# Optimization experiments

Hardware: AMD Instinct MI355X
Metric: run time of the kernel (lower is better)

The kernel has to match this reference:

```python
import jax, jax.numpy as jnp
import numpy as np

VOCAB, D = 10000, 32
QUEUE_LEN = 100


def setup_inputs() -> dict:
    key = jax.random.key(0)
    ks = jax.random.split(key, 8)
    B, T = 64, 1024
    s = 0.1
    return dict(
        inputs=jax.random.randint(ks[0], (B, T), 0, 10000, dtype=jnp.int32),
        emb=jax.random.normal(ks[1], (VOCAB, D), dtype=jnp.float32) * s,
        k_lstm=jax.random.normal(ks[2], (D, 4 * D), dtype=jnp.float32) * s,
        rk_lstm=jax.random.normal(ks[3], (D, 4 * D), dtype=jnp.float32) * s,
        b_lstm=jnp.zeros((4 * D,), dtype=jnp.float32),
        W1=jax.random.normal(ks[4], (D, D), dtype=jnp.float32) * s,
        b1=jnp.zeros((D,), dtype=jnp.float32),
        W2=jax.random.normal(ks[5], (D, 1), dtype=jnp.float32) * s,
        b2=jnp.zeros((1,), dtype=jnp.float32),
    )


def _lstm(x, k, rk, b):
    # Keras LSTM, gate order [i, f, g(cell), o], sigmoid recurrent act, tanh act.
    B, T, D = x.shape
    xg = jnp.einsum('btd,de->bte', x, k) + b  # precompute input projections

    def step(carry, xg_t):
        h, c = carry
        z = xg_t + h @ rk
        i, f, g, o = jnp.split(z, 4, axis=-1)
        c = jax.nn.sigmoid(f) * c + jax.nn.sigmoid(i) * jnp.tanh(g)
        h = jax.nn.sigmoid(o) * jnp.tanh(c)
        return (h, c), h

    init = (jnp.zeros((B, D), x.dtype), jnp.zeros((B, D), x.dtype))
    _, hs = jax.lax.scan(step, init, jnp.swapaxes(xg, 0, 1))  # [T,B,D]
    return jnp.swapaxes(hs, 0, 1)  # [B,T,D]


def _zero_index_queue(x_ids):
    # Vectorized replacement of the (i,j) Python scan: last QUEUE_LEN positions
    # (row-major order) where token==0, as [QUEUE_LEN,2] int32, padded with -1.
    B, T = x_ids.shape
    flat = (x_ids == 0).reshape(-1)
    N = flat.shape[0]
    ridx = jnp.nonzero(flat[::-1], size=QUEUE_LEN, fill_value=-1)[0]
    pos = jnp.where(ridx >= 0, N - 1 - ridx, -1)[::-1]  # ascending, like deque
    ii = jnp.where(pos >= 0, pos // T, -1)
    jj = jnp.where(pos >= 0, pos % T, -1)
    return jnp.stack([ii, jj], axis=-1).astype(jnp.int32)


def _forward_float(x_ids, emb, k_lstm, rk_lstm, b_lstm, W1, b1, W2, b2):
    x = emb[x_ids]                                  # [B,T,D]
    h = _lstm(x, k_lstm, rk_lstm, b_lstm)           # [B,T,D]
    scores = jnp.einsum('btd,bsd->bts', h, h)       # unscaled dot attention
    attn = jax.nn.softmax(scores, axis=-1)
    ctx = jnp.einsum('bts,bsd->btd', attn, h)       # Keras Attention output
    y = jnp.einsum('btd,bte->bde', ctx, h)          # Dot(axes=(1,1)) -> [B,D,D]
    y = jax.nn.relu(y @ W1 + b1)
    return jax.nn.sigmoid(y @ W2 + b2)              # [B,D,1]


def reference(inputs, emb, k_lstm, rk_lstm, b_lstm, W1, b1, W2, b2):
    x_ids = jnp.where(inputs < VOCAB, inputs, 0)
    out = _forward_float(x_ids, emb, k_lstm, rk_lstm, b_lstm, W1, b1, W2, b2)
    return out, _zero_index_queue(x_ids)
```

## Files before the change

kernel.cpp:

```cpp
#include <hip/hip_runtime.h>
#include <math.h>

#define BB 64
#define TT 1024
#define DD 32
#define GG 128
#define VOCABN 10000
#define QLEN 100

typedef short short8 __attribute__((ext_vector_type(8)));
typedef float floatx4 __attribute__((ext_vector_type(4)));
typedef float floatx2 __attribute__((ext_vector_type(2)));
typedef unsigned short u16;

__device__ __forceinline__ float fsig(float x) {
    return __builtin_amdgcn_rcpf(1.0f + __expf(-x));
}
__device__ __forceinline__ float readlane_f(float v, int l) {
    return __int_as_float(__builtin_amdgcn_readlane(__float_as_int(v), l));
}
__device__ __forceinline__ u16 f2bf_rne(float x) {
    unsigned u = __float_as_uint(x);
    u += 0x7FFF + ((u >> 16) & 1);
    return (u16)(u >> 16);
}
__device__ __forceinline__ float bf2f(u16 s) {
    return __uint_as_float(((unsigned)s) << 16);
}
__device__ __forceinline__ floatx2 fma2(float s, floatx2 w, floatx2 acc) {
    return __builtin_elementwise_fma((floatx2){s, s}, w, acc);
}

#define UU 8
__global__
__attribute__((amdgpu_flat_work_group_size(128, 128)))
__attribute__((amdgpu_waves_per_eu(1, 1)))
void k_lstm_scan(const int* __restrict__ ids,
                 const float* __restrict__ emb,
                 const float* __restrict__ klstm,
                 const float* __restrict__ bias,
                 const float* __restrict__ rk,
                 float* __restrict__ hout,
                 u16* __restrict__ hh, u16* __restrict__ hl,
                 u16* __restrict__ th, u16* __restrict__ tl,
                 int* __restrict__ list,
                 float* __restrict__ outq) {
    const int b = blockIdx.x;
    const int tid = threadIdx.x;
    const int wv = tid >> 6;
    const int l = tid & 63;
    if (b >= BB) {
        if (wv != 0) return;
        const int4* v4 = (const int4*)ids;
        const int C4 = (BB * TT) / 4 / 64;
        const int b4 = l * C4;
        int cnt = 0;
#pragma unroll 4
        for (int i = 0; i < C4; ++i) {
            int4 v = v4[b4 + i];
            cnt += (v.x == 0 || (unsigned)v.x >= VOCABN);
            cnt += (v.y == 0 || (unsigned)v.y >= VOCABN);
            cnt += (v.z == 0 || (unsigned)v.z >= VOCABN);
            cnt += (v.w == 0 || (unsigned)v.w >= VOCABN);
        }
        int scan = cnt;
#pragma unroll
        for (int o = 1; o < 64; o <<= 1) {
            int nn = __shfl_up(scan, o);
            if (l >= o) scan += nn;
        }
        const int total = __shfl(scan, 63);
        int off = scan - cnt;
        const int base = l * (C4 * 4);
#pragma unroll 4
        for (int i = 0; i < C4; ++i) {
            int4 v = v4[b4 + i];
            if (v.x == 0 || (unsigned)v.x >= VOCABN) list[off++] = base + 4 * i;
            if (v.y == 0 || (unsigned)v.y >= VOCABN) list[off++] = base + 4 * i + 1;
            if (v.z == 0 || (unsigned)v.z >= VOCABN) list[off++] = base + 4 * i + 2;
            if (v.w == 0 || (unsigned)v.w >= VOCABN) list[off++] = base + 4 * i + 3;
        }
        __threadfence();
        const int Kc = total < QLEN ? total : QLEN;
        for (int t = l; t < QLEN; t += 64) {
            float ii = -1.0f, jj = -1.0f;
            if (t >= QLEN - Kc) {
                int pos = list[total - QLEN + t];
                ii = (float)(pos >> 10);
                jj = (float)(pos & (TT - 1));
            }
            outq[2 * t] = ii;
            outq[2 * t + 1] = jj;
        }
        return;
    }

    __shared__ float ring[2][UU][GG];
    __shared__ __align__(16) float hring[2][UU][DD];
    const int* idsb = ids + b * TT;

    if (wv == 1) {
        const int ja = l, jb = l + 64;
        floatx2 kp[DD];
#pragma unroll
        for (int d2 = 0; d2 < DD; ++d2)
            kp[d2] = (floatx2){klstm[d2 * GG + ja], klstm[d2 * GG + jb]};
        const floatx2 bj = (floatx2){bias[ja], bias[jb]};
        const int dd = l & 31;
        const int u_r = l >> 3, dc = (l & 7) * 4;
        const int d_c = l & 31, ug = (l >> 5) * 4;
        u16* hhb = hh + (size_t)b * TT * DD;
        u16* hlb = hl + (size_t)b * TT * DD;
        u16* thb = th + (size_t)b * DD * TT;
        u16* tlb = tl + (size_t)b * DD * TT;

#define PROD_TOKEN(SEL, U, EV)                                               \
        {                                                                    \
            floatx2 z0 = bj;                                                 \
            floatx2 z1 = {0.f, 0.f}, z2 = {0.f, 0.f}, z3 = {0.f, 0.f};       \
            _Pragma("unroll")                                                \
            for (int k = 0; k < DD; k += 4) {                                \
                float e0 = readlane_f(EV, k);                                \
                float e1 = readlane_f(EV, k + 1);                            \
                float e2 = readlane_f(EV, k + 2);                            \
                float e3 = readlane_f(EV, k + 3);                            \
                z0 = fma2(e0, kp[k], z0);                                    \
                z1 = fma2(e1, kp[k + 1], z1);                                \
                z2 = fma2(e2, kp[k + 2], z2);                                \
                z3 = fma2(e3, kp[k + 3], z3);                                \
            }                                                                \
            floatx2 zf = (z0 + z1) + (z2 + z3);                              \
            ring[SEL][U][ja] = zf.x;                                         \
            ring[SEL][U][jb] = zf.y;                                         \
        }

#define CVT_CHUNK(HSEL, TC0)                                                 \
        {                                                                    \
            const float4 hv4 = *(const float4*)&hring[HSEL][u_r][dc];        \
            float xr[4] = {hv4.x, hv4.y, hv4.z, hv4.w};                      \
            u16 rh[4], rl[4];                                                \
            _Pragma("unroll")                                                \
            for (int i = 0; i < 4; ++i) {                                    \
                rh[i] = f2bf_rne(xr[i]);                                     \
                rl[i] = f2bf_rne(xr[i] - bf2f(rh[i]));                       \
            }                                                                \
            ushort4 rhv = {rh[0], rh[1], rh[2], rh[3]};                      \
            ushort4 rlv = {rl[0], rl[1], rl[2], rl[3]};                      \
            *(ushort4*)&hhb[(size_t)((TC0) + u_r) * DD + dc] = rhv;          \
            *(ushort4*)&hlb[(size_t)((TC0) + u_r) * DD + dc] = rlv;          \
            u16 ch[4], cl[4];                                                \
            _Pragma("unroll")                                                \
            for (int j = 0; j < 4; ++j) {                                    \
                float x = hring[HSEL][ug + j][d_c];                          \
                ch[j] = f2bf_rne(x);                                         \
                cl[j] = f2bf_rne(x - bf2f(ch[j]));                           \
            }                                                                \
            ushort4 chv = {ch[0], ch[1], ch[2], ch[3]};                      \
            ushort4 clv = {cl[0], cl[1], cl[2], cl[3]};                      \
            *(ushort4*)&thb[(size_t)d_c * TT + (TC0) + ug] = chv;            \
            *(ushort4*)&tlb[(size_t)d_c * TT + (TC0) + ug] = clv;            \
        }

        {
            int id0 = idsb[0]; if ((unsigned)id0 >= VOCABN) id0 = 0;
            float ec = emb[id0 * DD + dd];
#pragma unroll
            for (int u = 0; u < UU; ++u) {
                float en = 0.f;
                if (u + 1 < UU) {
                    int idn = idsb[u + 1]; if ((unsigned)idn >= VOCABN) idn = 0;
                    en = emb[idn * DD + dd];
                }
                PROD_TOKEN(0, u, ec)
                ec = en;
            }
        }
        __syncthreads();
        int sel = 0;
        for (int t0 = 0; t0 < TT; t0 += UU) {
            if (t0 + UU < TT) {
                const int s = sel ^ 1;
                int id0 = idsb[t0 + UU]; if ((unsigned)id0 >= VOCABN) id0 = 0;
                float ec = emb[id0 * DD + dd];
#pragma unroll
                for (int u = 0; u < UU; ++u) {
                    float en = 0.f;
                    if (u + 1 < UU) {
                        int tn = t0 + UU + u + 1;
                        if (tn > TT - 1) tn = TT - 1;
                        int idn = idsb[tn]; if ((unsigned)idn >= VOCABN) idn = 0;
                        en = emb[idn * DD + dd];
                    }
                    PROD_TOKEN(s, u, ec)
                    ec = en;
                }
            }
            if (t0) CVT_CHUNK((t0 / UU - 1) & 1, t0 - UU)
            __syncthreads();
            sel ^= 1;
        }
        CVT_CHUNK(1, TT - UU)
#undef PROD_TOKEN
#undef CVT_CHUNK
        return;
    }

    const int d = l & 31;
    const bool hi = l >= 32;
    const int ga = (hi ? 32 : 0) + d;
    const int gb = (hi ? 96 : 64) + d;
    floatx2 rkp[DD];
#pragma unroll
    for (int k = 0; k < DD; ++k)
        rkp[k] = (floatx2){rk[k * GG + ga], rk[k * GG + gb]};
    float* hb = hout + (size_t)b * TT * DD;

    float h = 0.0f, c = 0.0f;
    float hreg[UU];
    __syncthreads();
    int sel = 0;
    for (int t0 = 0; t0 < TT; t0 += UU) {
        if (t0 && !hi) {
#pragma unroll
            for (int u = 0; u < UU; ++u) hb[(size_t)(t0 - UU + u) * DD + d] = hreg[u];
        }
        float pa[UU], pb[UU];
#pragma unroll
        for (int u = 0; u < UU; ++u) {
            pa[u] = ring[sel][u][ga];
            pb[u] = ring[sel][u][gb];
        }
#pragma unroll
        for (int u = 0; u < UU; ++u) {
            floatx2 x0 = {pa[u], pb[u]};
            floatx2 x1 = {0.f, 0.f}, x2 = {0.f, 0.f}, x3 = {0.f, 0.f};
#pragma unroll
            for (int k = 0; k < DD; k += 4) {
                float h0 = readlane_f(h, k);
                float h1 = readlane_f(h, k + 1);
                float h2 = readlane_f(h, k + 2);
                float h3 = readlane_f(h, k + 3);
                x0 = fma2(h0, rkp[k],     x0);
                x1 = fma2(h1, rkp[k + 1], x1);
                x2 = fma2(h2, rkp[k + 2], x2);
                x3 = fma2(h3, rkp[k + 3], x3);
            }
            floatx2 zf = (x0 + x1) + (x2 + x3);
            float za = zf.x, zb = zf.y;
            float a = fsig(za);
            float zbm = hi ? zb : 2.0f * zb;
            float s2 = fsig(zbm);
            float bv = hi ? s2 : 2.0f * s2 - 1.0f;
            auto r1 = __builtin_amdgcn_permlane32_swap(
                __float_as_int(bv), __float_as_int(a), false, false);
            auto r2 = __builtin_amdgcn_permlane32_swap(
                __float_as_int(a), __float_as_int(bv), false, false);
            float fg = __int_as_float(r1[0]);
            float og = __int_as_float(r2[0]);
            c = fmaf(fg, c, a * bv);
            float tc = 2.0f * fsig(2.0f * c) - 1.0f;
            h = og * tc;
            hreg[u] = h;
            if (!hi) hring[sel][u][d] = h;
        }
        __syncthreads();
        sel ^= 1;
    }
    if (!hi) {
#pragma unroll
        for (int u = 0; u < UU; ++u) hb[(size_t)(TT - UU + u) * DD + d] = hreg[u];
    }
}

__global__ __launch_bounds__(256, 1) void k_attn(const u16* __restrict__ hh,
                                                 const u16* __restrict__ hl,
                                                 const u16* __restrict__ th,
                                                 const u16* __restrict__ tl,
                                                 u16* __restrict__ cth,
                                                 u16* __restrict__ ctl) {
    __shared__ u16 plds[4][4][2][16 * 40];
    __shared__ float ctile[4][64][34];
    const int tid = threadIdx.x;
    const int w = tid >> 6;
    const int l = tid & 63;
    const int m = l & 15;
    const int g = l >> 4;
    const int b = blockIdx.x & 63;
    const int qt = (blockIdx.x >> 6) * 4 + w;
    const int q0 = qt * 64;
    const size_t rb = (size_t)b * TT * DD;
    const size_t tb = (size_t)b * DD * TT;

    const short8 Qh0 = *(const short8*)&hh[rb + (size_t)(q0 + m) * DD + g * 8];
    const short8 Ql0 = *(const short8*)&hl[rb + (size_t)(q0 + m) * DD + g * 8];
    const short8 Qh1 = *(const short8*)&hh[rb + (size_t)(q0 + 16 + m) * DD + g * 8];
    const short8 Ql1 = *(const short8*)&hl[rb + (size_t)(q0 + 16 + m) * DD + g * 8];
    const short8 Qh2 = *(const short8*)&hh[rb + (size_t)(q0 + 32 + m) * DD + g * 8];
    const short8 Ql2 = *(const short8*)&hl[rb + (size_t)(q0 + 32 + m) * DD + g * 8];
    const short8 Qh3 = *(const short8*)&hh[rb + (size_t)(q0 + 48 + m) * DD + g * 8];
    const short8 Ql3 = *(const short8*)&hl[rb + (size_t)(q0 + 48 + m) * DD + g * 8];
    short8 ONES;
#pragma unroll
    for (int j = 0; j < 8; ++j) ONES[j] = (short)0x3F80;

    floatx4 c0 = {0.f, 0.f, 0.f, 0.f}, c1 = {0.f, 0.f, 0.f, 0.f};
    floatx4 c2 = {0.f, 0.f, 0.f, 0.f}, c3 = {0.f, 0.f, 0.f, 0.f};
    floatx4 c4 = {0.f, 0.f, 0.f, 0.f}, c5 = {0.f, 0.f, 0.f, 0.f};
    floatx4 c6 = {0.f, 0.f, 0.f, 0.f}, c7 = {0.f, 0.f, 0.f, 0.f};
    floatx4 la0 = {0.f, 0.f, 0.f, 0.f}, la1 = {0.f, 0.f, 0.f, 0.f};
    floatx4 la2 = {0.f, 0.f, 0.f, 0.f}, la3 = {0.f, 0.f, 0.f, 0.f};

#define S_BLOCK(QH, QL, KH_A, KL_A, KH_B, KL_B, SA, SB)                       \
    SA = __builtin_amdgcn_mfma_f32_16x16x32_bf16(QH, KH_A, SA, 0, 0, 0);      \
    SA = __builtin_amdgcn_mfma_f32_16x16x32_bf16(QH, KL_A, SA, 0, 0, 0);      \
    SA = __builtin_amdgcn_mfma_f32_16x16x32_bf16(QL, KH_A, SA, 0, 0, 0);      \
    SB = __builtin_amdgcn_mfma_f32_16x16x32_bf16(QH, KH_B, SB, 0, 0, 0);      \
    SB = __builtin_amdgcn_mfma_f32_16x16x32_bf16(QH, KL_B, SB, 0, 0, 0);      \
    SB = __builtin_amdgcn_mfma_f32_16x16x32_bf16(QL, KH_B, SB, 0, 0, 0);

#define EXP_STORE(SA, SB, TILE, SLOT)                                         \
    {                                                                         \
        u16* lp = plds[w][TILE][SLOT];                                        \
        _Pragma("unroll")                                                     \
        for (int r = 0; r < 4; ++r) {                                         \
            lp[(g * 4 + r) * 40 + m]      = f2bf_rne(__expf(SA[r]));          \
            lp[(g * 4 + r) * 40 + 16 + m] = f2bf_rne(__expf(SB[r]));          \
        }                                                                     \
    }

    {
        short8 KhA = *(const short8*)&hh[rb + (size_t)(m) * DD + g * 8];
        short8 KlA = *(const short8*)&hl[rb + (size_t)(m) * DD + g * 8];
        short8 KhB = *(const short8*)&hh[rb + (size_t)(16 + m) * DD + g * 8];
        short8 KlB = *(const short8*)&hl[rb + (size_t)(16 + m) * DD + g * 8];
        floatx4 sA = {0.f, 0.f, 0.f, 0.f}, sB = {0.f, 0.f, 0.f, 0.f};
        floatx4 tA = {0.f, 0.f, 0.f, 0.f}, tB = {0.f, 0.f, 0.f, 0.f};
        floatx4 uA = {0.f, 0.f, 0.f, 0.f}, uB = {0.f, 0.f, 0.f, 0.f};
        floatx4 vA = {0.f, 0.f, 0.f, 0.f}, vB = {0.f, 0.f, 0.f, 0.f};
        S_BLOCK(Qh0, Ql0, KhA, KlA, KhB, KlB, sA, sB)
        S_BLOCK(Qh1, Ql1, KhA, KlA, KhB, KlB, tA, tB)
        S_BLOCK(Qh2, Ql2, KhA, KlA, KhB, KlB, uA, uB)
        S_BLOCK(Qh3, Ql3, KhA, KlA, KhB, KlB, vA, vB)
        EXP_STORE(sA, sB, 0, 0)
        EXP_STORE(tA, tB, 1, 0)
        EXP_STORE(uA, uB, 2, 0)
        EXP_STORE(vA, vB, 3, 0)
    }
    short8 Vh0 = *(const short8*)&th[tb + (size_t)m * TT + g * 8];
    short8 Vl0 = *(const short8*)&tl[tb + (size_t)m * TT + g * 8];
    short8 Vh1 = *(const short8*)&th[tb + (size_t)(16 + m) * TT + g * 8];
    short8 Vl1 = *(const short8*)&tl[tb + (size_t)(16 + m) * TT + g * 8];
    short8 V2h0 = *(const short8*)&th[tb + (size_t)m * TT + 32 + g * 8];
    short8 V2l0 = *(const short8*)&tl[tb + (size_t)m * TT + 32 + g * 8];
    short8 V2h1 = *(const short8*)&th[tb + (size_t)(16 + m) * TT + 32 + g * 8];
    short8 V2l1 = *(const short8*)&tl[tb + (size_t)(16 + m) * TT + 32 + g * 8];
    short8 KhA = *(const short8*)&hh[rb + (size_t)(32 + m) * DD + g * 8];
    short8 KlA = *(const short8*)&hl[rb + (size_t)(32 + m) * DD + g * 8];
    short8 KhB = *(const short8*)&hh[rb + (size_t)(48 + m) * DD + g * 8];
    short8 KlB = *(const short8*)&hl[rb + (size_t)(48 + m) * DD + g * 8];
    short8 K2hA = *(const short8*)&hh[rb + (size_t)(64 + m) * DD + g * 8];
    short8 K2lA = *(const short8*)&hl[rb + (size_t)(64 + m) * DD + g * 8];
    short8 K2hB = *(const short8*)&hh[rb + (size_t)(80 + m) * DD + g * 8];
    short8 K2lB = *(const short8*)&hl[rb + (size_t)(80 + m) * DD + g * 8];

#pragma unroll 1
    for (int kp = 1; kp < 32; ++kp) {
        const int knK = (kp < 30) ? (kp + 2) * 32 : 0;
        const int knV = (kp < 31) ? (kp + 1) * 32 : 0;
        short8 nKhA = *(const short8*)&hh[rb + (size_t)(knK + m) * DD + g * 8];
        short8 nKlA = *(const short8*)&hl[rb + (size_t)(knK + m) * DD + g * 8];
        short8 nKhB = *(const short8*)&hh[rb + (size_t)(knK + 16 + m) * DD + g * 8];
        short8 nKlB = *(const short8*)&hl[rb + (size_t)(knK + 16 + m) * DD + g * 8];
        short8 nVh0 = *(const short8*)&th[tb + (size_t)m * TT + knV + g * 8];
        short8 nVl0 = *(const short8*)&tl[tb + (size_t)m * TT + knV + g * 8];
        short8 nVh1 = *(const short8*)&th[tb + (size_t)(16 + m) * TT + knV + g * 8];
        short8 nVl1 = *(const short8*)&tl[tb + (size_t)(16 + m) * TT + knV + g * 8];

        floatx4 sA = {0.f, 0.f, 0.f, 0.f}, sB = {0.f, 0.f, 0.f, 0.f};
        floatx4 tA = {0.f, 0.f, 0.f, 0.f}, tB = {0.f, 0.f, 0.f, 0.f};
        floatx4 uA = {0.f, 0.f, 0.f, 0.f}, uB = {0.f, 0.f, 0.f, 0.f};
        floatx4 vA = {0.f, 0.f, 0.f, 0.f}, vB = {0.f, 0.f, 0.f, 0.f};
        S_BLOCK(Qh0, Ql0, KhA, KlA, KhB, KlB, sA, sB)
        S_BLOCK(Qh1, Ql1, KhA, KlA, KhB, KlB, tA, tB)
        S_BLOCK(Qh2, Ql2, KhA, KlA, KhB, KlB, uA, uB)
        S_BLOCK(Qh3, Ql3, KhA, KlA, KhB, KlB, vA, vB)

        const int ps = (kp - 1) & 1;
        const short8 P0 = *(const short8*)&plds[w][0][ps][m * 40 + g * 8];
        const short8 P1 = *(const short8*)&plds[w][1][ps][m * 40 + g * 8];
        const short8 P2 = *(const short8*)&plds[w][2][ps][m * 40 + g * 8];
        const short8 P3 = *(const short8*)&plds[w][3][ps][m * 40 + g * 8];

        c0  = __builtin_amdgcn_mfma_f32_16x16x32_bf16(P0, Vh0, c0, 0, 0, 0);
        c0  = __builtin_amdgcn_mfma_f32_16x16x32_bf16(P0, Vl0, c0, 0, 0, 0);
        c1  = __builtin_amdgcn_mfma_f32_16x16x32_bf16(P0, Vh1, c1, 0, 0, 0);
        c1  = __builtin_amdgcn_mfma_f32_16x16x32_bf16(P0, Vl1, c1, 0, 0, 0);
        la0 = __builtin_amdgcn_mfma_f32_16x16x32_bf16(P0, ONES, la0, 0, 0, 0);
        c2  = __builtin_amdgcn_mfma_f32_16x16x32_bf16(P1, Vh0, c2, 0, 0, 0);
        c2  = __builtin_amdgcn_mfma_f32_16x16x32_bf16(P1, Vl0, c2, 0, 0, 0);
        c3  = __builtin_amdgcn_mfma_f32_16x16x32_bf16(P1, Vh1, c3, 0, 0, 0);
        c3  = __builtin_amdgcn_mfma_f32_16x16x32_bf16(P1, Vl1, c3, 0, 0, 0);
        la1 = __builtin_amdgcn_mfma_f32_16x16x32_bf16(P1, ONES, la1, 0, 0, 0);
        c4  = __builtin_amdgcn_mfma_f32_16x16x32_bf16(P2, Vh0, c4, 0, 0, 0);
        c4  = __builtin_amdgcn_mfma_f32_16x16x32_bf16(P2, Vl0, c4, 0, 0, 0);
        c5  = __builtin_amdgcn_mfma_f32_16x16x32_bf16(P2, Vh1, c5, 0, 0, 0);
        c5  = __builtin_amdgcn_mfma_f32_16x16x32_bf16(P2, Vl1, c5, 0, 0, 0);
        la2 = __builtin_amdgcn_mfma_f32_16x16x32_bf16(P2, ONES, la2, 0, 0, 0);
        c6  = __builtin_amdgcn_mfma_f32_16x16x32_bf16(P3, Vh0, c6, 0, 0, 0);
        c6  = __builtin_amdgcn_mfma_f32_16x16x32_bf16(P3, Vl0, c6, 0, 0, 0);
        c7  = __builtin_amdgcn_mfma_f32_16x16x32_bf16(P3, Vh1, c7, 0, 0, 0);
        c7  = __builtin_amdgcn_mfma_f32_16x16x32_bf16(P3, Vl1, c7, 0, 0, 0);
        la3 = __builtin_amdgcn_mfma_f32_16x16x32_bf16(P3, ONES, la3, 0, 0, 0);

        EXP_STORE(sA, sB, 0, kp & 1)
        EXP_STORE(tA, tB, 1, kp & 1)
        EXP_STORE(uA, uB, 2, kp & 1)
        EXP_STORE(vA, vB, 3, kp & 1)

        KhA = K2hA; KlA = K2lA; KhB = K2hB; KlB = K2lB;
        K2hA = nKhA; K2lA = nKlA; K2hB = nKhB; K2lB = nKlB;
        Vh0 = V2h0; Vl0 = V2l0; Vh1 = V2h1; Vl1 = V2l1;
        V2h0 = nVh0; V2l0 = nVl0; V2h1 = nVh1; V2l1 = nVl1;
    }
    {
        const short8 P0 = *(const short8*)&plds[w][0][1][m * 40 + g * 8];
        const short8 P1 = *(const short8*)&plds[w][1][1][m * 40 + g * 8];
        const short8 P2 = *(const short8*)&plds[w][2][1][m * 40 + g * 8];
        const short8 P3 = *(const short8*)&plds[w][3][1][m * 40 + g * 8];
        c0  = __builtin_amdgcn_mfma_f32_16x16x32_bf16(P0, Vh0, c0, 0, 0, 0);
        c0  = __builtin_amdgcn_mfma_f32_16x16x32_bf16(P0, Vl0, c0, 0, 0, 0);
        c1  = __builtin_amdgcn_mfma_f32_16x16x32_bf16(P0, Vh1, c1, 0, 0, 0);
        c1  = __builtin_amdgcn_mfma_f32_16x16x32_bf16(P0, Vl1, c1, 0, 0, 0);
        la0 = __builtin_amdgcn_mfma_f32_16x16x32_bf16(P0, ONES, la0, 0, 0, 0);
        c2  = __builtin_amdgcn_mfma_f32_16x16x32_bf16(P1, Vh0, c2, 0, 0, 0);
        c2  = __builtin_amdgcn_mfma_f32_16x16x32_bf16(P1, Vl0, c2, 0, 0, 0);
        c3  = __builtin_amdgcn_mfma_f32_16x16x32_bf16(P1, Vh1, c3, 0, 0, 0);
        c3  = __builtin_amdgcn_mfma_f32_16x16x32_bf16(P1, Vl1, c3, 0, 0, 0);
        la1 = __builtin_amdgcn_mfma_f32_16x16x32_bf16(P1, ONES, la1, 0, 0, 0);
        c4  = __builtin_amdgcn_mfma_f32_16x16x32_bf16(P2, Vh0, c4, 0, 0, 0);
        c4  = __builtin_amdgcn_mfma_f32_16x16x32_bf16(P2, Vl0, c4, 0, 0, 0);
        c5  = __builtin_amdgcn_mfma_f32_16x16x32_bf16(P2, Vh1, c5, 0, 0, 0);
        c5  = __builtin_amdgcn_mfma_f32_16x16x32_bf16(P2, Vl1, c5, 0, 0, 0);
        la2 = __builtin_amdgcn_mfma_f32_16x16x32_bf16(P2, ONES, la2, 0, 0, 0);
        c6  = __builtin_amdgcn_mfma_f32_16x16x32_bf16(P3, Vh0, c6, 0, 0, 0);
        c6  = __builtin_amdgcn_mfma_f32_16x16x32_bf16(P3, Vl0, c6, 0, 0, 0);
        c7  = __builtin_amdgcn_mfma_f32_16x16x32_bf16(P3, Vh1, c7, 0, 0, 0);
        c7  = __builtin_amdgcn_mfma_f32_16x16x32_bf16(P3, Vl1, c7, 0, 0, 0);
        la3 = __builtin_amdgcn_mfma_f32_16x16x32_bf16(P3, ONES, la3, 0, 0, 0);
    }
#undef S_BLOCK
#undef EXP_STORE
#pragma unroll
    for (int r = 0; r < 4; ++r) {
        float li0 = __builtin_amdgcn_rcpf(la0[r]);
        float li1 = __builtin_amdgcn_rcpf(la1[r]);
        float li2 = __builtin_amdgcn_rcpf(la2[r]);
        float li3 = __builtin_amdgcn_rcpf(la3[r]);
        ctile[w][g * 4 + r][m]            = c0[r] * li0;
        ctile[w][g * 4 + r][16 + m]       = c1[r] * li0;
        ctile[w][16 + g * 4 + r][m]       = c2[r] * li1;
        ctile[w][16 + g * 4 + r][16 + m]  = c3[r] * li1;
        ctile[w][32 + g * 4 + r][m]       = c4[r] * li2;
        ctile[w][32 + g * 4 + r][16 + m]  = c5[r] * li2;
        ctile[w][48 + g * 4 + r][m]       = c6[r] * li3;
        ctile[w][48 + g * 4 + r][16 + m]  = c7[r] * li3;
    }
    const int srow = l >> 3;
    const int tcol = (l & 7) * 8;
#pragma unroll
    for (int cblk = 0; cblk < 4; ++cblk) {
        const int dr = cblk * 8 + srow;
        short8 hvec, lvec;
#pragma unroll
        for (int j2 = 0; j2 < 8; ++j2) {
            float v = ctile[w][tcol + j2][dr];
            u16 hv = f2bf_rne(v);
            hvec[j2] = (short)hv;
            lvec[j2] = (short)f2bf_rne(v - bf2f(hv));
        }
        *(short8*)&cth[tb + (size_t)dr * TT + q0 + tcol] = hvec;
        *(short8*)&ctl[tb + (size_t)dr * TT + q0 + tcol] = lvec;
    }
}

__global__ __launch_bounds__(256) void k_ymlp(const u16* __restrict__ cth,
                                              const u16* __restrict__ ctl,
                                              const u16* __restrict__ th,
                                              const u16* __restrict__ tl,
                                              const float* __restrict__ W1,
                                              const float* __restrict__ b1,
                                              const float* __restrict__ W2,
                                              const float* __restrict__ b2,
                                              float* __restrict__ out) {
    const int b = blockIdx.x;
    const int tid = threadIdx.x;
    const int w = tid >> 6;
    const int l = tid & 63;
    const int m = l & 15;
    const int g = l >> 4;
    const size_t tb = (size_t)b * DD * TT;
    const int k0 = w * (TT / 4);

    floatx4 y00 = {0.f, 0.f, 0.f, 0.f}, y01 = {0.f, 0.f, 0.f, 0.f};
    floatx4 y10 = {0.f, 0.f, 0.f, 0.f}, y11 = {0.f, 0.f, 0.f, 0.f};
#pragma unroll 2
    for (int ks = 0; ks < TT / 4; ks += 32) {
        const size_t kk = (size_t)(k0 + ks + g * 8);
        short8 A0h = *(const short8*)&cth[tb + (size_t)m * TT + kk];
        short8 A0l = *(const short8*)&ctl[tb + (size_t)m * TT + kk];
        short8 A1h = *(const short8*)&cth[tb + (size_t)(16 + m) * TT + kk];
        short8 A1l = *(const short8*)&ctl[tb + (size_t)(16 + m) * TT + kk];
        short8 B0h = *(const short8*)&th[tb + (size_t)m * TT + kk];
        short8 B0l = *(const short8*)&tl[tb + (size_t)m * TT + kk];
        short8 B1h = *(const short8*)&th[tb + (size_t)(16 + m) * TT + kk];
        short8 B1l = *(const short8*)&tl[tb + (size_t)(16 + m) * TT + kk];
        y00 = __builtin_amdgcn_mfma_f32_16x16x32_bf16(A0h, B0h, y00, 0, 0, 0);
        y00 = __builtin_amdgcn_mfma_f32_16x16x32_bf16(A0h, B0l, y00, 0, 0, 0);
        y00 = __builtin_amdgcn_mfma_f32_16x16x32_bf16(A0l, B0h, y00, 0, 0, 0);
        y01 = __builtin_amdgcn_mfma_f32_16x16x32_bf16(A0h, B1h, y01, 0, 0, 0);
        y01 = __builtin_amdgcn_mfma_f32_16x16x32_bf16(A0h, B1l, y01, 0, 0, 0);
        y01 = __builtin_amdgcn_mfma_f32_16x16x32_bf16(A0l, B1h, y01, 0, 0, 0);
        y10 = __builtin_amdgcn_mfma_f32_16x16x32_bf16(A1h, B0h, y10, 0, 0, 0);
        y10 = __builtin_amdgcn_mfma_f32_16x16x32_bf16(A1h, B0l, y10, 0, 0, 0);
        y10 = __builtin_amdgcn_mfma_f32_16x16x32_bf16(A1l, B0h, y10, 0, 0, 0);
        y11 = __builtin_amdgcn_mfma_f32_16x16x32_bf16(A1h, B1h, y11, 0, 0, 0);
        y11 = __builtin_amdgcn_mfma_f32_16x16x32_bf16(A1h, B1l, y11, 0, 0, 0);
        y11 = __builtin_amdgcn_mfma_f32_16x16x32_bf16(A1l, B1h, y11, 0, 0, 0);
    }
    __shared__ float ysp[4][DD][DD];
#pragma unroll
    for (int r = 0; r < 4; ++r) {
        ysp[w][g * 4 + r][m]           = y00[r];
        ysp[w][g * 4 + r][16 + m]      = y01[r];
        ysp[w][16 + g * 4 + r][m]      = y10[r];
        ysp[w][16 + g * 4 + r][16 + m] = y11[r];
    }
    __syncthreads();
    const int e = tid & 31;
    const int d4 = (tid >> 5) * 4;
    __shared__ float ys[DD][DD];
#pragma unroll
    for (int r = 0; r < 4; ++r)
        ys[d4 + r][e] = (ysp[0][d4 + r][e] + ysp[1][d4 + r][e])
                      + (ysp[2][d4 + r][e] + ysp[3][d4 + r][e]);
    __syncthreads();
    __shared__ float yr[DD][33];
#pragma unroll
    for (int r = 0; r < 4; ++r) {
        float v = b1[e];
#pragma unroll
        for (int ee = 0; ee < DD; ++ee) v += ys[d4 + r][ee] * W1[ee * DD + e];
        yr[d4 + r][e] = fmaxf(v, 0.0f);
    }
    __syncthreads();
    if (tid < DD) {
        float v = b2[0];
#pragma unroll
        for (int ee = 0; ee < DD; ++ee) v += yr[tid][ee] * W2[ee];
        out[b * DD + tid] = 1.0f / (1.0f + expf(-v));
    }
}

extern "C" void kernel_launch(void* const* d_in, const int* in_sizes, int n_in,
                              void* d_out, int out_size, void* d_ws, size_t ws_size,
                              hipStream_t stream) {
    const int* ids   = (const int*)d_in[0];
    const float* emb = (const float*)d_in[1];
    const float* kl  = (const float*)d_in[2];
    const float* rk  = (const float*)d_in[3];
    const float* bl  = (const float*)d_in[4];
    const float* W1  = (const float*)d_in[5];
    const float* b1  = (const float*)d_in[6];
    const float* W2  = (const float*)d_in[7];
    const float* b2  = (const float*)d_in[8];
    float* out = (float*)d_out;

    char* ws = (char*)d_ws;
    const size_t H_ELEMS = (size_t)BB * TT * DD;
    u16* hh   = (u16*)ws;
    u16* hl   = (u16*)(ws + H_ELEMS * 2);
    u16* th   = (u16*)(ws + H_ELEMS * 4);
    u16* tl   = (u16*)(ws + H_ELEMS * 6);
    float* h  = (float*)(ws + H_ELEMS * 8);
    u16* cth  = (u16*)(ws + H_ELEMS * 8 + H_ELEMS * 4);
    u16* ctl  = (u16*)(ws + H_ELEMS * 8 + H_ELEMS * 4 + H_ELEMS * 2);
    int* list = (int*)(ws + H_ELEMS * 8 + H_ELEMS * 8);

    k_lstm_scan<<<BB + 1, 128, 0, stream>>>(ids, emb, kl, bl, rk, h,
                                            hh, hl, th, tl, list, out + BB * DD);
    k_attn<<<BB * 4, 256, 0, stream>>>(hh, hl, th, tl, cth, ctl);
    k_ymlp<<<BB, 256, 0, stream>>>(cth, ctl, th, tl, W1, b1, W2, b2, out);
}
```

Baseline: 358.1 us.

## Drop unused fp32 h store from LSTM and widen attention key panels to 64

The LSTM scan no longer writes an fp32 copy of h to global memory, since downstream kernels only read the bf16 hi/lo split versions. The attention kernel now handles 64 keys per loop iteration as two 32-key panels, with double-buffered P tiles in one shared-memory array that is reused for the context tile. This halves the loop trip count and gives more independent MFMA work between loads, at the cost of more registers for the prefetched K and V.

```diff
diff --git a/kernel.cpp b/kernel.cpp
--- a/kernel.cpp
+++ b/kernel.cpp
@@ -40,7 +40,6 @@
                  const float* __restrict__ klstm,
                  const float* __restrict__ bias,
                  const float* __restrict__ rk,
-                 float* __restrict__ hout,
                  u16* __restrict__ hh, u16* __restrict__ hl,
                  u16* __restrict__ th, u16* __restrict__ tl,
                  int* __restrict__ list,
@@ -213,17 +212,11 @@
 #pragma unroll
     for (int k = 0; k < DD; ++k)
         rkp[k] = (floatx2){rk[k * GG + ga], rk[k * GG + gb]};
-    float* hb = hout + (size_t)b * TT * DD;
 
     float h = 0.0f, c = 0.0f;
-    float hreg[UU];
     __syncthreads();
     int sel = 0;
     for (int t0 = 0; t0 < TT; t0 += UU) {
-        if (t0 && !hi) {
-#pragma unroll
-            for (int u = 0; u < UU; ++u) hb[(size_t)(t0 - UU + u) * DD + d] = hreg[u];
-        }
         float pa[UU], pb[UU];
 #pragma unroll
         for (int u = 0; u < UU; ++u) {
@@ -260,15 +253,10 @@
             c = fmaf(fg, c, a * bv);
             float tc = 2.0f * fsig(2.0f * c) - 1.0f;
             h = og * tc;
-            hreg[u] = h;
             if (!hi) hring[sel][u][d] = h;
         }
         __syncthreads();
         sel ^= 1;
-    }
-    if (!hi) {
-#pragma unroll
-        for (int u = 0; u < UU; ++u) hb[(size_t)(TT - UU + u) * DD + d] = hreg[u];
     }
 }
 
@@ -278,8 +266,7 @@
                                                  const u16* __restrict__ tl,
                                                  u16* __restrict__ cth,
                                                  u16* __restrict__ ctl) {
-    __shared__ u16 plds[4][4][2][16 * 40];
-    __shared__ float ctile[4][64][34];
+    __shared__ __align__(16) char smem[4][20480];
     const int tid = threadIdx.x;
     const int w = tid >> 6;
     const int l = tid & 63;
@@ -290,6 +277,7 @@
     const int q0 = qt * 64;
     const size_t rb = (size_t)b * TT * DD;
     const size_t tb = (size_t)b * DD * TT;
+    u16* plw = (u16*)smem[w];
 
     const short8 Qh0 = *(const short8*)&hh[rb + (size_t)(q0 + m) * DD + g * 8];
     const short8 Ql0 = *(const short8*)&hl[rb + (size_t)(q0 + m) * DD + g * 8];
@@ -318,9 +306,9 @@
     SB = __builtin_amdgcn_mfma_f32_16x16x32_bf16(QH, KL_B, SB, 0, 0, 0);      \
     SB = __builtin_amdgcn_mfma_f32_16x16x32_bf16(QL, KH_B, SB, 0, 0, 0);
 
-#define EXP_STORE(SA, SB, TILE, SLOT)                                         \
+#define EXP_STORE(SA, SB, TILE, SLOT, PN)                                     \
     {                                                                         \
-        u16* lp = plds[w][TILE][SLOT];                                        \
+        u16* lp = plw + (((TILE) * 2 + (SLOT)) * 2 + (PN)) * 640;             \
         _Pragma("unroll")                                                     \
         for (int r = 0; r < 4; ++r) {                                         \
             lp[(g * 4 + r) * 40 + m]      = f2bf_rne(__expf(SA[r]));          \
@@ -328,142 +316,113 @@
         }                                                                     \
     }
 
+#define SPANEL(KhA, KlA, KhB, KlB, SLOT, PN)                                  \
+    {                                                                         \
+        floatx4 sA = {0.f, 0.f, 0.f, 0.f}, sB = {0.f, 0.f, 0.f, 0.f};         \
+        floatx4 tA = {0.f, 0.f, 0.f, 0.f}, tB = {0.f, 0.f, 0.f, 0.f};         \
+        floatx4 uA = {0.f, 0.f, 0.f, 0.f}, uB = {0.f, 0.f, 0.f, 0.f};         \
+        floatx4 vA = {0.f, 0.f, 0.f, 0.f}, vB = {0.f, 0.f, 0.f, 0.f};         \
+        S_BLOCK(Qh0, Ql0, KhA, KlA, KhB, KlB, sA, sB)                         \
+        S_BLOCK(Qh1, Ql1, KhA, KlA, KhB, KlB, tA, tB)                         \
+        S_BLOCK(Qh2, Ql2, KhA, KlA, KhB, KlB, uA, uB)                         \
+        S_BLOCK(Qh3, Ql3, KhA, KlA, KhB, KlB, vA, vB)                         \
+        EXP_STORE(sA, sB, 0, SLOT, PN)                                        \
+        EXP_STORE(tA, tB, 1, SLOT, PN)                                        \
+        EXP_STORE(uA, uB, 2, SLOT, PN)                                        \
+        EXP_STORE(vA, vB, 3, SLOT, PN)                                        \
+    }
+
+#define PV_TILE(T, CA, CB, LAc, SLOTP, PN, VH0, VL0, VH1, VL1)                \
+    {                                                                         \
+        const short8 P = *(const short8*)&plw[(((T) * 2 + (SLOTP)) * 2 + (PN)) * 640 + m * 40 + g * 8]; \
+        CA  = __builtin_amdgcn_mfma_f32_16x16x32_bf16(P, VH0, CA, 0, 0, 0);   \
+        CA  = __builtin_amdgcn_mfma_f32_16x16x32_bf16(P, VL0, CA, 0, 0, 0);   \
+        CB  = __builtin_amdgcn_mfma_f32_16x16x32_bf16(P, VH1, CB, 0, 0, 0);   \
+        CB  = __builtin_amdgcn_mfma_f32_16x16x32_bf16(P, VL1, CB, 0, 0, 0);   \
+        LAc = __builtin_amdgcn_mfma_f32_16x16x32_bf16(P, ONES, LAc, 0, 0, 0); \
+    }
+
+#define PV_PANEL(SLOTP, PN, VH0, VL0, VH1, VL1)                               \
+    PV_TILE(0, c0, c1, la0, SLOTP, PN, VH0, VL0, VH1, VL1)                    \
+    PV_TILE(1, c2, c3, la1, SLOTP, PN, VH0, VL0, VH1, VL1)                    \
+    PV_TILE(2, c4, c5, la2, SLOTP, PN, VH0, VL0, VH1, VL1)                    \
+    PV_TILE(3, c6, c7, la3, SLOTP, PN, VH0, VL0, VH1, VL1)
+
+#define LOAD_K(BASE, RA, RLA, RB, RLB)                                        \
+    RA  = *(const short8*)&hh[rb + (size_t)((BASE) + m) * DD + g * 8];        \
+    RLA = *(const short8*)&hl[rb + (size_t)((BASE) + m) * DD + g * 8];        \
+    RB  = *(const short8*)&hh[rb + (size_t)((BASE) + 16 + m) * DD + g * 8];   \
+    RLB = *(const short8*)&hl[rb + (size_t)((BASE) + 16 + m) * DD + g * 8];
+
+#define LOAD_V(BASE, RH0, RL0, RH1, RL1)                                      \
+    RH0 = *(const short8*)&th[tb + (size_t)m * TT + (BASE) + g * 8];          \
+    RL0 = *(const short8*)&tl[tb + (size_t)m * TT + (BASE) + g * 8];          \
+    RH1 = *(const short8*)&th[tb + (size_t)(16 + m) * TT + (BASE) + g * 8];   \
+    RL1 = *(const short8*)&tl[tb + (size_t)(16 + m) * TT + (BASE) + g * 8];
+
     {
-        short8 KhA = *(const short8*)&hh[rb + (size_t)(m) * DD + g * 8];
-        short8 KlA = *(const short8*)&hl[rb + (size_t)(m) * DD + g * 8];
-        short8 KhB = *(const short8*)&hh[rb + (size_t)(16 + m) * DD + g * 8];
-        short8 KlB = *(const short8*)&hl[rb + (size_t)(16 + m) * DD + g * 8];
-        floatx4 sA = {0.f, 0.f, 0.f, 0.f}, sB = {0.f, 0.f, 0.f, 0.f};
-        floatx4 tA = {0.f, 0.f, 0.f, 0.f}, tB = {0.f, 0.f, 0.f, 0.f};
-        floatx4 uA = {0.f, 0.f, 0.f, 0.f}, uB = {0.f, 0.f, 0.f, 0.f};
-        floatx4 vA = {0.f, 0.f, 0.f, 0.f}, vB = {0.f, 0.f, 0.f, 0.f};
-        S_BLOCK(Qh0, Ql0, KhA, KlA, KhB, KlB, sA, sB)
-        S_BLOCK(Qh1, Ql1, KhA, KlA, KhB, KlB, tA, tB)
-        S_BLOCK(Qh2, Ql2, KhA, KlA, KhB, KlB, uA, uB)
-        S_BLOCK(Qh3, Ql3, KhA, KlA, KhB, KlB, vA, vB)
-        EXP_STORE(sA, sB, 0, 0)
-        EXP_STORE(tA, tB, 1, 0)
-        EXP_STORE(uA, uB, 2, 0)
-        EXP_STORE(vA, vB, 3, 0)
-    }
-    short8 Vh0 = *(const short8*)&th[tb + (size_t)m * TT + g * 8];
-    short8 Vl0 = *(const short8*)&tl[tb + (size_t)m * TT + g * 8];
-    short8 Vh1 = *(const short8*)&th[tb + (size_t)(16 + m) * TT + g * 8];
-    short8 Vl1 = *(const short8*)&tl[tb + (size_t)(16 + m) * TT + g * 8];
-    short8 V2h0 = *(const short8*)&th[tb + (size_t)m * TT + 32 + g * 8];
-    short8 V2l0 = *(const short8*)&tl[tb + (size_t)m * TT + 32 + g * 8];
-    short8 V2h1 = *(const short8*)&th[tb + (size_t)(16 + m) * TT + 32 + g * 8];
-    short8 V2l1 = *(const short8*)&tl[tb + (size_t)(16 + m) * TT + 32 + g * 8];
-    short8 KhA = *(const short8*)&hh[rb + (size_t)(32 + m) * DD + g * 8];
-    short8 KlA = *(const short8*)&hl[rb + (size_t)(32 + m) * DD + g * 8];
-    short8 KhB = *(const short8*)&hh[rb + (size_t)(48 + m) * DD + g * 8];
-    short8 KlB = *(const short8*)&hl[rb + (size_t)(48 + m) * DD + g * 8];
-    short8 K2hA = *(const short8*)&hh[rb + (size_t)(64 + m) * DD + g * 8];
-    short8 K2lA = *(const short8*)&hl[rb + (size_t)(64 + m) * DD + g * 8];
-    short8 K2hB = *(const short8*)&hh[rb + (size_t)(80 + m) * DD + g * 8];
-    short8 K2lB = *(const short8*)&hl[rb + (size_t)(80 + m) * DD + g * 8];
+        short8 KA, KLA, KB, KLB;
+        LOAD_K(0, KA, KLA, KB, KLB)
+        SPANEL(KA, KLA, KB, KLB, 0, 0)
+        LOAD_K(32, KA, KLA, KB, KLB)
+        SPANEL(KA, KLA, KB, KLB, 0, 1)
+    }
+    short8 V0h0, V0l0, V0h1, V0l1, V1h0, V1l0, V1h1, V1l1;
+    short8 K0hA, K0lA, K0hB, K0lB, K1hA, K1lA, K1hB, K1lB;
+    LOAD_V(0,  V0h0, V0l0, V0h1, V0l1)
+    LOAD_V(32, V1h0, V1l0, V1h1, V1l1)
+    LOAD_K(64, K0hA, K0lA, K0hB, K0lB)
+    LOAD_K(96, K1hA, K1lA, K1hB, K1lB)
 
 #pragma unroll 1
-    for (int kp = 1; kp < 32; ++kp) {
-        const int knK = (kp < 30) ? (kp + 2) * 32 : 0;
-        const int knV = (kp < 31) ? (kp + 1) * 32 : 0;
-        short8 nKhA = *(const short8*)&hh[rb + (size_t)(knK + m) * DD + g * 8];
-        short8 nKlA = *(const short8*)&hl[rb + (size_t)(knK + m) * DD + g * 8];
-        short8 nKhB = *(const short8*)&hh[rb + (size_t)(knK + 16 + m) * DD + g * 8];
-        short8 nKlB = *(const short8*)&hl[rb + (size_t)(knK + 16 + m) * DD + g * 8];
-        short8 nVh0 = *(const short8*)&th[tb + (size_t)m * TT + knV + g * 8];
-        short8 nVl0 = *(const short8*)&tl[tb + (size_t)m * TT + knV + g * 8];
-        short8 nVh1 = *(const short8*)&th[tb + (size_t)(16 + m) * TT + knV + g * 8];
-        short8 nVl1 = *(const short8*)&tl[tb + (size_t)(16 + m) * TT + knV + g * 8];
-
-        floatx4 sA = {0.f, 0.f, 0.f, 0.f}, sB = {0.f, 0.f, 0.f, 0.f};
-        floatx4 tA = {0.f, 0.f, 0.f, 0.f}, tB = {0.f, 0.f, 0.f, 0.f};
-        floatx4 uA = {0.f, 0.f, 0.f, 0.f}, uB = {0.f, 0.f, 0.f, 0.f};
-        floatx4 vA = {0.f, 0.f, 0.f, 0.f}, vB = {0.f, 0.f, 0.f, 0.f};
-        S_BLOCK(Qh0, Ql0, KhA, KlA, KhB, KlB, sA, sB)
-        S_BLOCK(Qh1, Ql1, KhA, KlA, KhB, KlB, tA, tB)
-        S_BLOCK(Qh2, Ql2, KhA, KlA, KhB, KlB, uA, uB)
-        S_BLOCK(Qh3, Ql3, KhA, KlA, KhB, KlB, vA, vB)
-
-        const int ps = (kp - 1) & 1;
-        const short8 P0 = *(const short8*)&plds[w][0][ps][m * 40 + g * 8];
-        const short8 P1 = *(const short8*)&plds[w][1][ps][m * 40 + g * 8];
-        const short8 P2 = *(const short8*)&plds[w][2][ps][m * 40 + g * 8];
-        const short8 P3 = *(const short8*)&plds[w][3][ps][m * 40 + g * 8];
-
-        c0  = __builtin_amdgcn_mfma_f32_16x16x32_bf16(P0, Vh0, c0, 0, 0, 0);
-        c0  = __builtin_amdgcn_mfma_f32_16x16x32_bf16(P0, Vl0, c0, 0, 0, 0);
-        c1  = __builtin_amdgcn_mfma_f32_16x16x32_bf16(P0, Vh1, c1, 0, 0, 0);
-        c1  = __builtin_amdgcn_mfma_f32_16x16x32_bf16(P0, Vl1, c1, 0, 0, 0);
-        la0 = __builtin_amdgcn_mfma_f32_16x16x32_bf16(P0, ONES, la0, 0, 0, 0);
-        c2  = __builtin_amdgcn_mfma_f32_16x16x32_bf16(P1, Vh0, c2, 0, 0, 0);
-        c2  = __builtin_amdgcn_mfma_f32_16x16x32_bf16(P1, Vl0, c2, 0, 0, 0);
-        c3  = __builtin_amdgcn_mfma_f32_16x16x32_bf16(P1, Vh1, c3, 0, 0, 0);
-        c3  = __builtin_amdgcn_mfma_f32_16x16x32_bf16(P1, Vl1, c3, 0, 0, 0);
-        la1 = __builtin_amdgcn_mfma_f32_16x16x32_bf16(P1, ONES, la1, 0, 0, 0);
-        c4  = __builtin_amdgcn_mfma_f32_16x16x32_bf16(P2, Vh0, c4, 0, 0, 0);
-        c4  = __builtin_amdgcn_mfma_f32_16x16x32_bf16(P2, Vl0, c4, 0, 0, 0);
-        c5  = __builtin_amdgcn_mfma_f32_16x16x32_bf16(P2, Vh1, c5, 0, 0, 0);
-        c5  = __builtin_amdgcn_mfma_f32_16x16x32_bf16(P2, Vl1, c5, 0, 0, 0);
-        la2 = __builtin_amdgcn_mfma_f32_16x16x32_bf16(P2, ONES, la2, 0, 0, 0);
-        c6  = __builtin_amdgcn_mfma_f32_16x16x32_bf16(P3, Vh0, c6, 0, 0, 0);
-        c6  = __builtin_amdgcn_mfma_f32_16x16x32_bf16(P3, Vl0, c6, 0, 0, 0);
-        c7  = __builtin_amdgcn_mfma_f32_16x16x32_bf16(P3, Vh1, c7, 0, 0, 0);
-        c7  = __builtin_amdgcn_mfma_f32_16x16x32_bf16(P3, Vl1, c7, 0, 0, 0);
-        la3 = __builtin_amdgcn_mfma_f32_16x16x32_bf16(P3, ONES, la3, 0, 0, 0);
-
-        EXP_STORE(sA, sB, 0, kp & 1)
-        EXP_STORE(tA, tB, 1, kp & 1)
-        EXP_STORE(uA, uB, 2, kp & 1)
-        EXP_STORE(vA, vB, 3, kp & 1)
-
-        KhA = K2hA; KlA = K2lA; KhB = K2hB; KlB = K2lB;
-        K2hA = nKhA; K2lA = nKlA; K2hB = nKhB; K2lB = nKlB;
-        Vh0 = V2h0; Vl0 = V2l0; Vh1 = V2h1; Vl1 = V2l1;
-        V2h0 = nVh0; V2l0 = nVl0; V2h1 = nVh1; V2l1 = nVl1;
-    }
-    {
-        const short8 P0 = *(const short8*)&plds[w][0][1][m * 40 + g * 8];
-        const short8 P1 = *(const short8*)&plds[w][1][1][m * 40 + g * 8];
-        const short8 P2 = *(const short8*)&plds[w][2][1][m * 40 + g * 8];
-        const short8 P3 = *(const short8*)&plds[w][3][1][m * 40 + g * 8];
-        c0  = __builtin_amdgcn_mfma_f32_16x16x32_bf16(P0, Vh0, c0, 0, 0, 0);
-        c0  = __builtin_amdgcn_mfma_f32_16x16x32_bf16(P0, Vl0, c0, 0, 0, 0);
-        c1  = __builtin_amdgcn_mfma_f32_16x16x32_bf16(P0, Vh1, c1, 0, 0, 0);
-        c1  = __builtin_amdgcn_mfma_f32_16x16x32_bf16(P0, Vl1, c1, 0, 0, 0);
-        la0 = __builtin_amdgcn_mfma_f32_16x16x32_bf16(P0, ONES, la0, 0, 0, 0);
-        c2  = __builtin_amdgcn_mfma_f32_16x16x32_bf16(P1, Vh0, c2, 0, 0, 0);
-        c2  = __builtin_amdgcn_mfma_f32_16x16x32_bf16(P1, Vl0, c2, 0, 0, 0);
-        c3  = __builtin_amdgcn_mfma_f32_16x16x32_bf16(P1, Vh1, c3, 0, 0, 0);
-        c3  = __builtin_amdgcn_mfma_f32_16x16x32_bf16(P1, Vl1, c3, 0, 0, 0);
-        la1 = __builtin_amdgcn_mfma_f32_16x16x32_bf16(P1, ONES, la1, 0, 0, 0);
-        c4  = __builtin_amdgcn_mfma_f32_16x16x32_bf16(P2, Vh0, c4, 0, 0, 0);
-        c4  = __builtin_amdgcn_mfma_f32_16x16x32_bf16(P2, Vl0, c4, 0, 0, 0);
-        c5  = __builtin_amdgcn_mfma_f32_16x16x32_bf16(P2, Vh1, c5, 0, 0, 0);
-        c5  = __builtin_amdgcn_mfma_f32_16x16x32_bf16(P2, Vl1, c5, 0, 0, 0);
-        la2 = __builtin_amdgcn_mfma_f32_16x16x32_bf16(P2, ONES, la2, 0, 0, 0);
-        c6  = __builtin_amdgcn_mfma_f32_16x16x32_bf16(P3, Vh0, c6, 0, 0, 0);
-        c6  = __builtin_amdgcn_mfma_f32_16x16x32_bf16(P3, Vl0, c6, 0, 0, 0);
-        c7  = __builtin_amdgcn_mfma_f32_16x16x32_bf16(P3, Vh1, c7, 0, 0, 0);
-        c7  = __builtin_amdgcn_mfma_f32_16x16x32_bf16(P3, Vl1, c7, 0, 0, 0);
-        la3 = __builtin_amdgcn_mfma_f32_16x16x32_bf16(P3, ONES, la3, 0, 0, 0);
-    }
+    for (int j = 1; j < 16; ++j) {
+        const int kb = (j < 15) ? 64 * (j + 1) : 0;
+        const int vb = 64 * j;
+        short8 nK0hA, nK0lA, nK0hB, nK0lB, nK1hA, nK1lA, nK1hB, nK1lB;
+        short8 nV0h0, nV0l0, nV0h1, nV0l1, nV1h0, nV1l0, nV1h1, nV1l1;
+        LOAD_K(kb,      nK0hA, nK0lA, nK0hB, nK0lB)
+        LOAD_K(kb + 32, nK1hA, nK1lA, nK1hB, nK1lB)
+        LOAD_V(vb,      nV0h0, nV0l0, nV0h1, nV0l1)
+        LOAD_V(vb + 32, nV1h0, nV1l0, nV1h1, nV1l1)
+
+        const int sl = j & 1;
+        SPANEL(K0hA, K0lA, K0hB, K0lB, sl, 0)
+        SPANEL(K1hA, K1lA, K1hB, K1lB, sl, 1)
+
+        const int sp = (j - 1) & 1;
+        PV_PANEL(sp, 0, V0h0, V0l0, V0h1, V0l1)
+        PV_PANEL(sp, 1, V1h0, V1l0, V1h1, V1l1)
+
+        K0hA = nK0hA; K0lA = nK0lA; K0hB = nK0hB; K0lB = nK0lB;
+        K1hA = nK1hA; K1lA = nK1lA; K1hB = nK1hB; K1lB = nK1lB;
+        V0h0 = nV0h0; V0l0 = nV0l0; V0h1 = nV0h1; V0l1 = nV0l1;
+        V1h0 = nV1h0; V1l0 = nV1l0; V1h1 = nV1h1; V1l1 = nV1l1;
+    }
+    PV_PANEL(1, 0, V0h0, V0l0, V0h1, V0l1)
+    PV_PANEL(1, 1, V1h0, V1l0, V1h1, V1l1)
 #undef S_BLOCK
 #undef EXP_STORE
+#undef SPANEL
+#undef PV_TILE
+#undef PV_PANEL
+#undef LOAD_K
+#undef LOAD_V
+
+    float (*ct)[34] = (float (*)[34])smem[w];
 #pragma unroll
     for (int r = 0; r < 4; ++r) {
         float li0 = __builtin_amdgcn_rcpf(la0[r]);
         float li1 = __builtin_amdgcn_rcpf(la1[r]);
         float li2 = __builtin_amdgcn_rcpf(la2[r]);
         float li3 = __builtin_amdgcn_rcpf(la3[r]);
-        ctile[w][g * 4 + r][m]            = c0[r] * li0;
-        ctile[w][g * 4 + r][16 + m]       = c1[r] * li0;
-        ctile[w][16 + g * 4 + r][m]       = c2[r] * li1;
-        ctile[w][16 + g * 4 + r][16 + m]  = c3[r] * li1;
-        ctile[w][32 + g * 4 + r][m]       = c4[r] * li2;
-        ctile[w][32 + g * 4 + r][16 + m]  = c5[r] * li2;
-        ctile[w][48 + g * 4 + r][m]       = c6[r] * li3;
-        ctile[w][48 + g * 4 + r][16 + m]  = c7[r] * li3;
+        ct[g * 4 + r][m]            = c0[r] * li0;
+        ct[g * 4 + r][16 + m]       = c1[r] * li0;
+        ct[16 + g * 4 + r][m]       = c2[r] * li1;
+        ct[16 + g * 4 + r][16 + m]  = c3[r] * li1;
+        ct[32 + g * 4 + r][m]       = c4[r] * li2;
+        ct[32 + g * 4 + r][16 + m]  = c5[r] * li2;
+        ct[48 + g * 4 + r][m]       = c6[r] * li3;
+        ct[48 + g * 4 + r][16 + m]  = c7[r] * li3;
     }
     const int srow = l >> 3;
     const int tcol = (l & 7) * 8;
@@ -473,7 +432,7 @@
         short8 hvec, lvec;
 #pragma unroll
         for (int j2 = 0; j2 < 8; ++j2) {
-            float v = ctile[w][tcol + j2][dr];
+            float v = ct[tcol + j2][dr];
             u16 hv = f2bf_rne(v);
             hvec[j2] = (short)hv;
             lvec[j2] = (short)f2bf_rne(v - bf2f(hv));
@@ -581,12 +540,11 @@
     u16* hl   = (u16*)(ws + H_ELEMS * 2);
     u16* th   = (u16*)(ws + H_ELEMS * 4);
     u16* tl   = (u16*)(ws + H_ELEMS * 6);
-    float* h  = (float*)(ws + H_ELEMS * 8);
     u16* cth  = (u16*)(ws + H_ELEMS * 8 + H_ELEMS * 4);
     u16* ctl  = (u16*)(ws + H_ELEMS * 8 + H_ELEMS * 4 + H_ELEMS * 2);
     int* list = (int*)(ws + H_ELEMS * 8 + H_ELEMS * 8);
 
-    k_lstm_scan<<<BB + 1, 128, 0, stream>>>(ids, emb, kl, bl, rk, h,
+    k_lstm_scan<<<BB + 1, 128, 0, stream>>>(ids, emb, kl, bl, rk,
                                             hh, hl, th, tl, list, out + BB * DD);
     k_attn<<<BB * 4, 256, 0, stream>>>(hh, hl, th, tl, cth, ctl);
     k_ymlp<<<BB, 256, 0, stream>>>(cth, ctl, th, tl, W1, b1, W2, b2, out);
```

After: 358.9 us. About the same (+0.2%).
